# Kernel tuning notes

Hardware: AMD Instinct MI355X
Metric: run time of the kernel (lower is better)

The kernel has to match this reference:

```python
import jax, jax.numpy as jnp
import numpy as np

NUM_GRAPHS = 500


def setup_inputs() -> dict:
    key = jax.random.key(0)
    ks = jax.random.split(key, 8)
    num_nodes, feat, S, R, num_edges = 50000, 16, 128, 4, 1600000
    x = jax.random.normal(ks[0], (num_nodes, feat), dtype=jnp.float32)
    edge_index = jax.random.randint(ks[1], (2, num_edges), 0, num_nodes, dtype=jnp.int64)
    batch = jnp.sort(jax.random.randint(ks[2], (num_nodes,), 0, NUM_GRAPHS, dtype=jnp.int64))
    # ensure num_graphs == NUM_GRAPHS deterministically
    batch = batch.at[-1].set(NUM_GRAPHS - 1)
    scale = 1.0 / np.sqrt(S)
    W_msg = jax.random.uniform(ks[3], (R, S, S), jnp.float32, -scale, scale)
    b_msg = jax.random.uniform(ks[4], (R, S), jnp.float32, -scale, scale)
    W_upd = jax.random.uniform(ks[5], (R, S, S), jnp.float32, -scale, scale)
    b_upd = jax.random.uniform(ks[6], (R, S), jnp.float32, -scale, scale)
    return {"x": x, "W_msg": W_msg, "b_msg": b_msg, "W_upd": W_upd, "b_upd": b_upd,
            "edge_index": edge_index, "batch": batch}


def reference(x, W_msg, b_msg, W_upd, b_upd, edge_index, batch):
    num_nodes = x.shape[0]
    R, S, _ = W_msg.shape
    src, dst = edge_index[0], edge_index[1]
    # Original torch code initializes state to zeros (input_net is unused in forward).
    state = jnp.zeros((num_nodes, S), dtype=x.dtype)
    for r in range(R):
        message = jax.nn.relu(state @ W_msg[r].T + b_msg[r])          # [N, S]
        gathered = message[src]                                        # [E, S] gather
        agg = jnp.zeros((num_nodes, S), dtype=x.dtype).at[dst].add(gathered)  # scatter-add
        state = state + jax.nn.relu(agg @ W_upd[r].T + b_upd[r])
    graph_state = jax.ops.segment_sum(state, batch, num_segments=NUM_GRAPHS)  # [G, S]
    return graph_state
```

## Files before the change

kernel.cpp:

```cpp
#include <hip/hip_runtime.h>
#include <hip/hip_bf16.h>
#include <cstdint>
#include <cstddef>

#define SDIM 128
#define EPB2 4096
#define BCAP 4608

typedef short bf16x8 __attribute__((ext_vector_type(8)));
typedef float f32x4 __attribute__((ext_vector_type(4)));

__device__ __forceinline__ unsigned short f2bf(float f) {
  unsigned int u = __float_as_uint(f);
  unsigned int r = (u + 0x7FFF + ((u >> 16) & 1)) >> 16;
  return (unsigned short)r;
}
__device__ __forceinline__ float bf2f(unsigned short b) {
  return __uint_as_float(((unsigned int)b) << 16);
}

__global__ __launch_bounds__(256) void bucket_k(const int* __restrict__ src,
                                                const int* __restrict__ dst,
                                                int* __restrict__ bcursor,
                                                unsigned int* __restrict__ pairBuf4,
                                                int E) {
  __shared__ unsigned int s_buf[EPB2];
  __shared__ int cnt[512], base[512], gbase[512];
  const int tid = threadIdx.x;
  const int e0 = blockIdx.x * EPB2;
  const int n = min(EPB2, E - e0);
  cnt[tid] = 0; cnt[tid + 256] = 0;
  __syncthreads();

  unsigned int pack_r[16];
  int rank_r[16], bkt_r[16];
  if (n == EPB2) {
    const int4* dp = (const int4*)(dst + e0 + tid * 16);
    const int4* sp = (const int4*)(src + e0 + tid * 16);
#pragma unroll
    for (int q = 0; q < 4; ++q) {
      const int4 dv = dp[q];
      const int4 sv = sp[q];
      const int dd[4] = {dv.x, dv.y, dv.z, dv.w};
      const int ss[4] = {sv.x, sv.y, sv.z, sv.w};
#pragma unroll
      for (int w = 0; w < 4; ++w) {
        const int u = q * 4 + w;
        const int b = dd[w] >> 7;
        bkt_r[u] = b;
        pack_r[u] = ((unsigned int)dd[w] << 16) | (unsigned int)ss[w];
        rank_r[u] = atomicAdd(&cnt[b], 1);
      }
    }
  } else {
#pragma unroll
    for (int u = 0; u < 16; ++u) {
      const int li = u * 256 + tid;
      bkt_r[u] = -1;
      if (li < n) {
        const int i = e0 + li;
        const int d = dst[i];
        const int b = d >> 7;
        bkt_r[u] = b;
        pack_r[u] = ((unsigned int)d << 16) | (unsigned int)src[i];
        rank_r[u] = atomicAdd(&cnt[b], 1);
      }
    }
  }
  __syncthreads();
  if (tid < 64) {
    int carry = 0;
#pragma unroll
    for (int chunk = 0; chunk < 512; chunk += 256) {
      const int j0 = chunk + tid * 4;
      const int c0 = cnt[j0], c1 = cnt[j0 + 1], c2 = cnt[j0 + 2], c3 = cnt[j0 + 3];
      const int s = c0 + c1 + c2 + c3;
      int incl = s;
#pragma unroll
      for (int off = 1; off < 64; off <<= 1) {
        int u = __shfl_up(incl, off, 64);
        if (tid >= off) incl += u;
      }
      const int e = carry + incl - s;
      base[j0] = e;
      base[j0 + 1] = e + c0;
      base[j0 + 2] = e + c0 + c1;
      base[j0 + 3] = e + c0 + c1 + c2;
      carry += __shfl(incl, 63, 64);
    }
  }
  __syncthreads();
  for (int b = tid; b < 512; b += 256)
    if (cnt[b] > 0) gbase[b] = atomicAdd(&bcursor[b], cnt[b]);
  __syncthreads();
#pragma unroll
  for (int u = 0; u < 16; ++u) {
    if (n == EPB2 || bkt_r[u] >= 0)
      s_buf[base[bkt_r[u]] + rank_r[u]] = pack_r[u];
  }
  __syncthreads();
  for (int i = tid; i < n; i += 256) {
    const unsigned int p = s_buf[i];
    const int b = (int)(p >> 23);
    pairBuf4[(size_t)b * BCAP + (size_t)(gbase[b] + (i - base[b]))] = p;
  }
}

__global__ __launch_bounds__(512) void fill3_k(const unsigned int* __restrict__ pairBuf4,
                                               const int* __restrict__ bcursor,
                                               int* __restrict__ offs,
                                               int* __restrict__ oend,
                                               unsigned short* __restrict__ csr, int N) {
  const int b = blockIdx.x;
  const int rlo = b * BCAP;
  const int rhi = rlo + bcursor[b];
  const int lo_node = b << 7;
  __shared__ int hist[128], cur[128];
  const int tid = threadIdx.x;
  if (tid < 128) hist[tid] = 0;
  __syncthreads();
  for (int i = rlo + tid; i < rhi; i += 512)
    atomicAdd(&hist[(pairBuf4[i] >> 16) & 127], 1);
  __syncthreads();
  if (tid < 64) {
    const int j0 = tid * 2;
    const int h0 = hist[j0], h1 = hist[j0 + 1];
    const int s = h0 + h1;
    int incl = s;
#pragma unroll
    for (int off = 1; off < 64; off <<= 1) {
      int u = __shfl_up(incl, off, 64);
      if (tid >= off) incl += u;
    }
    const int e = rlo + incl - s;
    cur[j0] = e; cur[j0 + 1] = e + h0;
    const int n0 = lo_node + j0;
    if (n0 < N) { offs[n0] = e; oend[n0] = e + h0; }
    if (n0 + 1 < N) { offs[n0 + 1] = e + h0; oend[n0 + 1] = e + h0 + h1; }
  }
  __syncthreads();
  for (int i = rlo + tid; i < rhi; i += 512) {
    const unsigned int p = pairBuf4[i];
    const int pos = atomicAdd(&cur[(p >> 16) & 127], 1);
    csr[pos] = (unsigned short)p;
  }
}

__global__ __launch_bounds__(256) void cast2c_k(const float* __restrict__ a,
                                                const float* __restrict__ b,
                                                unsigned short* __restrict__ out, int n,
                                                const float* __restrict__ W_upd0,
                                                const float* __restrict__ b_msg0,
                                                float* __restrict__ cvec, int nCast) {
  if ((int)blockIdx.x == nCast) {
    __shared__ float m0[SDIM];
    const int j = threadIdx.x;
    if (j < SDIM) m0[j] = fmaxf(b_msg0[j], 0.f);
    __syncthreads();
    if (j < SDIM) {
      float s = 0.f;
      const float* wr = W_upd0 + (size_t)j * SDIM;
      for (int k = 0; k < SDIM; ++k) s += wr[k] * m0[k];
      cvec[j] = s;
    }
    return;
  }
  int i = (blockIdx.x * 256 + threadIdx.x) * 4;
  if (i >= 2 * n) return;
  const float* s = (i < n) ? (a + i) : (b + (i - n));
  float4 v = *(const float4*)s;
  ushort4 o;
  o.x = f2bf(v.x); o.y = f2bf(v.y); o.z = f2bf(v.z); o.w = f2bf(v.w);
  *(ushort4*)(out + i) = o;
}

__global__ __launch_bounds__(256) void initmsg_k(const int* __restrict__ offs,
                                                 const int* __restrict__ oend,
                                                 const float* __restrict__ cvec,
                                                 const float* __restrict__ bu0,
                                                 const unsigned short* __restrict__ Wm,
                                                 const float* __restrict__ bm,
                                                 unsigned short* __restrict__ sbf,
                                                 unsigned short* __restrict__ msgb, int N) {
  __shared__ unsigned short sT[4][16][136];
  const int tid = threadIdx.x, lane = tid & 63, wid = tid >> 6;
  const int r0 = blockIdx.x * 64 + wid * 16;
  int arow = r0 + (lane & 15);
  const bool rowOk = arow < N;
  if (!rowOk) arow = N - 1;
  const int kb = (lane >> 4) * 8;
  const float dn = (float)(oend[arow] - offs[arow]);

  bf16x8 a[4];
#pragma unroll
  for (int ks = 0; ks < 4; ++ks) {
    const int c0 = ks * 32 + kb;
#pragma unroll
    for (int q = 0; q < 8; ++q) {
      const float v = fmaxf(dn * cvec[c0 + q] + bu0[c0 + q], 0.f);
      a[ks][q] = (short)f2bf(v);
    }
    if (rowOk) *(bf16x8*)(sbf + (size_t)arow * SDIM + c0) = a[ks];
  }

  f32x4 acc[8];
#pragma unroll
  for (int jt = 0; jt < 8; ++jt) acc[jt] = (f32x4){0.f, 0.f, 0.f, 0.f};
  const int wrow = lane & 15;
#pragma unroll
  for (int ks = 0; ks < 4; ++ks) {
#pragma unroll
    for (int jt = 0; jt < 8; ++jt) {
      bf16x8 b = *(const bf16x8*)(Wm + (size_t)(jt * 16 + wrow) * SDIM + ks * 32 + kb);
      acc[jt] = __builtin_amdgcn_mfma_f32_16x16x32_bf16(a[ks], b, acc[jt], 0, 0, 0);
    }
  }
  const int colw = lane & 15;
  const int rt0 = (lane >> 4) * 4;
#pragma unroll
  for (int jt = 0; jt < 8; ++jt) {
    const float bj = bm[jt * 16 + colw];
#pragma unroll
    for (int r = 0; r < 4; ++r)
      sT[wid][rt0 + r][jt * 16 + colw] = f2bf(fmaxf(acc[jt][r] + bj, 0.f));
  }
  __syncthreads();
  const int vr = lane >> 4;
  const int vc = (lane & 15) * 8;
#pragma unroll
  for (int it = 0; it < 4; ++it) {
    const int lr = it * 4 + vr;
    const int row = r0 + lr;
    if (row < N)
      *(bf16x8*)(msgb + (size_t)row * SDIM + vc) = *(const bf16x8*)&sT[wid][lr][vc];
  }
}

template <bool MSG>
__global__ __launch_bounds__(256) void updmsg_k(const unsigned short* __restrict__ aggb,
                                                const unsigned short* __restrict__ Wu,
                                                const float* __restrict__ bu,
                                                unsigned short* __restrict__ sbf,
                                                const unsigned short* __restrict__ Wm,
                                                const float* __restrict__ bm,
                                                unsigned short* __restrict__ msgb, int N) {
  __shared__ unsigned short sT[4][16][136];
  const int tid = threadIdx.x, lane = tid & 63, wid = tid >> 6;
  const int r0 = blockIdx.x * 64 + wid * 16;
  int arow = r0 + (lane & 15);
  if (arow >= N) arow = N - 1;
  const int kb = (lane >> 4) * 8;

  f32x4 acc[8];
#pragma unroll
  for (int jt = 0; jt < 8; ++jt) acc[jt] = (f32x4){0.f, 0.f, 0.f, 0.f};
  bf16x8 a[4];
#pragma unroll
  for (int ks = 0; ks < 4; ++ks)
    a[ks] = *(const bf16x8*)(aggb + (size_t)arow * SDIM + ks * 32 + kb);
  const int wrow = lane & 15;
#pragma unroll
  for (int ks = 0; ks < 4; ++ks) {
#pragma unroll
    for (int jt = 0; jt < 8; ++jt) {
      bf16x8 b = *(const bf16x8*)(Wu + (size_t)(jt * 16 + wrow) * SDIM + ks * 32 + kb);
      acc[jt] = __builtin_amdgcn_mfma_f32_16x16x32_bf16(a[ks], b, acc[jt], 0, 0, 0);
    }
  }

  const int colw = lane & 15;
  const int rt0 = (lane >> 4) * 4;
#pragma unroll
  for (int jt = 0; jt < 8; ++jt) {
    const float bj = bu[jt * 16 + colw];
#pragma unroll
    for (int r = 0; r < 4; ++r)
      sT[wid][rt0 + r][jt * 16 + colw] = f2bf(fmaxf(acc[jt][r] + bj, 0.f));
  }
  __syncthreads();

  const int vr = lane >> 4;
  const int vc = (lane & 15) * 8;
#pragma unroll
  for (int it = 0; it < 4; ++it) {
    const int lr = it * 4 + vr;
    const int row = r0 + lr;
    if (row < N) {
      bf16x8 nw = *(const bf16x8*)&sT[wid][lr][vc];
      bf16x8 old = *(const bf16x8*)(sbf + (size_t)row * SDIM + vc);
      bf16x8 up;
#pragma unroll
      for (int q = 0; q < 8; ++q)
        up[q] = (short)f2bf(bf2f((unsigned short)old[q]) + bf2f((unsigned short)nw[q]));
      *(bf16x8*)(sbf + (size_t)row * SDIM + vc) = up;
      if (MSG) *(bf16x8*)&sT[wid][lr][vc] = up;
    }
  }

  if (MSG) {
    __syncthreads();
    f32x4 acc2[8];
#pragma unroll
    for (int jt = 0; jt < 8; ++jt) acc2[jt] = (f32x4){0.f, 0.f, 0.f, 0.f};
#pragma unroll
    for (int ks = 0; ks < 4; ++ks) {
      bf16x8 a2 = *(const bf16x8*)&sT[wid][lane & 15][ks * 32 + kb];
#pragma unroll
      for (int jt = 0; jt < 8; ++jt) {
        bf16x8 b = *(const bf16x8*)(Wm + (size_t)(jt * 16 + wrow) * SDIM + ks * 32 + kb);
        acc2[jt] = __builtin_amdgcn_mfma_f32_16x16x32_bf16(a2, b, acc2[jt], 0, 0, 0);
      }
    }
    __syncthreads();
#pragma unroll
    for (int jt = 0; jt < 8; ++jt) {
      const float bj = bm[jt * 16 + colw];
#pragma unroll
      for (int r = 0; r < 4; ++r)
        sT[wid][rt0 + r][jt * 16 + colw] = f2bf(fmaxf(acc2[jt][r] + bj, 0.f));
    }
    __syncthreads();
#pragma unroll
    for (int it = 0; it < 4; ++it) {
      const int lr = it * 4 + vr;
      const int row = r0 + lr;
      if (row < N)
        *(bf16x8*)(msgb + (size_t)row * SDIM + vc) = *(const bf16x8*)&sT[wid][lr][vc];
    }
  }
}

__global__ __launch_bounds__(256) void agg_bf16_k(const unsigned short* __restrict__ msg,
                                                  const unsigned short* __restrict__ csr,
                                                  const int* __restrict__ offs,
                                                  const int* __restrict__ oend,
                                                  unsigned short* __restrict__ aggb, int N) {
  const int wid = (blockIdx.x * 256 + threadIdx.x) >> 6;
  if (wid >= N) return;
  const int lane = threadIdx.x & 63;
  const int grp = lane >> 4;
  const unsigned int lb = (unsigned int)((lane & 15) << 4);
  const char* base = (const char*)msg;
  const int e1 = oend[wid];
  int e = offs[wid];
  float a0 = 0.f, a1 = 0.f, a2 = 0.f, a3 = 0.f, a4 = 0.f, a5 = 0.f, a6 = 0.f, a7 = 0.f;
#define ACC8(v) { \
  a0 += __uint_as_float((v).x << 16); a1 += __uint_as_float((v).x & 0xFFFF0000u); \
  a2 += __uint_as_float((v).y << 16); a3 += __uint_as_float((v).y & 0xFFFF0000u); \
  a4 += __uint_as_float((v).z << 16); a5 += __uint_as_float((v).z & 0xFFFF0000u); \
  a6 += __uint_as_float((v).w << 16); a7 += __uint_as_float((v).w & 0xFFFF0000u); }
  for (; e + 16 <= e1; e += 16) {
    const unsigned int o0 = ((unsigned int)csr[e + grp] << 8) | lb;
    const unsigned int o1 = ((unsigned int)csr[e + 4 + grp] << 8) | lb;
    const unsigned int o2 = ((unsigned int)csr[e + 8 + grp] << 8) | lb;
    const unsigned int o3 = ((unsigned int)csr[e + 12 + grp] << 8) | lb;
    uint4 vA = *(const uint4*)(base + o0);
    uint4 vB = *(const uint4*)(base + o1);
    uint4 vC = *(const uint4*)(base + o2);
    uint4 vD = *(const uint4*)(base + o3);
    ACC8(vA) ACC8(vB) ACC8(vC) ACC8(vD)
  }
  for (; e + 4 <= e1; e += 4) {
    const unsigned int o0 = ((unsigned int)csr[e + grp] << 8) | lb;
    uint4 v = *(const uint4*)(base + o0);
    ACC8(v)
  }
  if (e + grp < e1) {
    const unsigned int o0 = ((unsigned int)csr[e + grp] << 8) | lb;
    uint4 v = *(const uint4*)(base + o0);
    ACC8(v)
  }
#undef ACC8
#define RED(x) x += __shfl_xor(x, 16, 64); x += __shfl_xor(x, 32, 64);
  RED(a0) RED(a1) RED(a2) RED(a3) RED(a4) RED(a5) RED(a6) RED(a7)
#undef RED
  if (grp == 0) {
    uint4 o;
    o.x = (unsigned int)f2bf(a0) | ((unsigned int)f2bf(a1) << 16);
    o.y = (unsigned int)f2bf(a2) | ((unsigned int)f2bf(a3) << 16);
    o.z = (unsigned int)f2bf(a4) | ((unsigned int)f2bf(a5) << 16);
    o.w = (unsigned int)f2bf(a6) | ((unsigned int)f2bf(a7) << 16);
    *(uint4*)(aggb + ((size_t)wid << 7) + (lb >> 1)) = o;
  }
}

__global__ __launch_bounds__(SDIM) void segsum_k(const unsigned short* __restrict__ sbf,
                                                 const int* __restrict__ batch,
                                                 int N, float* __restrict__ out) {
  const int g = blockIdx.x;
  __shared__ int se[2];
  if (threadIdx.x < 2) {
    const int target = g + threadIdx.x;
    int lo = 0, hi = N;
    while (lo < hi) {
      const int mid = (lo + hi) >> 1;
      if (batch[mid] < target) lo = mid + 1; else hi = mid;
    }
    se[threadIdx.x] = lo;
  }
  __syncthreads();
  const int s = se[0], e = se[1];
  const int j = threadIdx.x;
  float acc = 0.f;
  for (int i = s; i < e; ++i) acc += bf2f(sbf[(size_t)i * SDIM + j]);
  out[(size_t)g * SDIM + j] = acc;
}

extern "C" void kernel_launch(void* const* d_in, const int* in_sizes, int n_in,
                              void* d_out, int out_size, void* d_ws, size_t ws_size,
                              hipStream_t stream) {
  const float* W_msg = (const float*)d_in[1];
  const float* b_msg = (const float*)d_in[2];
  const float* W_upd = (const float*)d_in[3];
  const float* b_upd = (const float*)d_in[4];
  const int* edges = (const int*)d_in[5];
  const int* batch = (const int*)d_in[6];
  const int E = in_sizes[5] / 2;
  const int N = in_sizes[6];
  const int G = out_size / SDIM;
  const int R = in_sizes[2] / SDIM;
  const int WSZ = R * SDIM * SDIM;

  const int NB = (N + 127) >> 7;

  const size_t NS = (size_t)N * SDIM;
  unsigned short* sbf = (unsigned short*)d_ws;
  unsigned short* msgb = sbf + NS;
  unsigned short* aggb = msgb + NS;
  unsigned short* wmsgb = aggb + NS;
  unsigned short* wupdb = wmsgb + WSZ;
  float* cvec = (float*)(wupdb + WSZ);
  int* offs = (int*)(cvec + SDIM);
  int* oend = offs + N;
  int* bcursor = oend + N;
  unsigned int* pairBuf4 = (unsigned int*)(bcursor + NB);
  unsigned short* csr = (unsigned short*)(pairBuf4 + (size_t)NB * BCAP);

  const int* srcArr = edges;
  const int* dstArr = edges + E;

  hipMemsetAsync(bcursor, 0, sizeof(int) * (size_t)NB, stream);

  const int nCast = (2 * WSZ / 4 + 255) / 256;
  cast2c_k<<<nCast + 1, 256, 0, stream>>>(W_msg, W_upd, wmsgb, WSZ,
                                          W_upd, b_msg, cvec, nCast);
  bucket_k<<<(E + EPB2 - 1) / EPB2, 256, 0, stream>>>(srcArr, dstArr, bcursor,
                                                      pairBuf4, E);
  fill3_k<<<NB, 512, 0, stream>>>(pairBuf4, bcursor, offs, oend, csr, N);

  const int gemmGrid = (N + 63) / 64;
  const int aggGrid = (N * 64 + 255) / 256;

  initmsg_k<<<gemmGrid, 256, 0, stream>>>(offs, oend, cvec, b_upd,
                                          wmsgb + (size_t)1 * SDIM * SDIM,
                                          b_msg + 1 * SDIM, sbf, msgb, N);
  agg_bf16_k<<<aggGrid, 256, 0, stream>>>(msgb, csr, offs, oend, aggb, N);
  for (int r = 1; r < R - 1; ++r) {
    updmsg_k<true><<<gemmGrid, 256, 0, stream>>>(
        aggb, wupdb + (size_t)r * SDIM * SDIM, b_upd + (size_t)r * SDIM, sbf,
        wmsgb + (size_t)(r + 1) * SDIM * SDIM, b_msg + (size_t)(r + 1) * SDIM, msgb, N);
    agg_bf16_k<<<aggGrid, 256, 0, stream>>>(msgb, csr, offs, oend, aggb, N);
  }
  updmsg_k<false><<<gemmGrid, 256, 0, stream>>>(
      aggb, wupdb + (size_t)(R - 1) * SDIM * SDIM, b_upd + (size_t)(R - 1) * SDIM, sbf,
      nullptr, nullptr, nullptr, N);

  segsum_k<<<G, SDIM, 0, stream>>>(sbf, batch, N, (float*)d_out);
}
```

Before: 340.2 us.

## Replace wavefront-per-node aggregation with thread-per-node column-sliced gather

The CSR gather-sum kernel changes from one 64-lane wavefront per destination node to one thread per node per 32-column slice. Each block handles one of four column slices and one half of the node range, and each thread keeps 32 fp32 accumulators in registers. This drops the cross-lane shuffle reduction and the index reads repeated across lane groups, and keeps each block's reads inside a 64-byte slice of the message rows, which may improve cache locality. In exchange, neighbouring lanes follow independent neighbour lists, so loads become uncoalesced and lanes diverge on uneven degrees, and register pressure rises.

Result: slower. 532.8 us (+56.6%).

```diff
diff --git a/kernel.cpp b/kernel.cpp
--- a/kernel.cpp
+++ b/kernel.cpp
@@ -330,57 +330,59 @@
   }
 }
 
-__global__ __launch_bounds__(256) void agg_bf16_k(const unsigned short* __restrict__ msg,
-                                                  const unsigned short* __restrict__ csr,
-                                                  const int* __restrict__ offs,
-                                                  const int* __restrict__ oend,
-                                                  unsigned short* __restrict__ aggb, int N) {
-  const int wid = (blockIdx.x * 256 + threadIdx.x) >> 6;
-  if (wid >= N) return;
-  const int lane = threadIdx.x & 63;
-  const int grp = lane >> 4;
-  const unsigned int lb = (unsigned int)((lane & 15) << 4);
-  const char* base = (const char*)msg;
-  const int e1 = oend[wid];
-  int e = offs[wid];
-  float a0 = 0.f, a1 = 0.f, a2 = 0.f, a3 = 0.f, a4 = 0.f, a5 = 0.f, a6 = 0.f, a7 = 0.f;
-#define ACC8(v) { \
-  a0 += __uint_as_float((v).x << 16); a1 += __uint_as_float((v).x & 0xFFFF0000u); \
-  a2 += __uint_as_float((v).y << 16); a3 += __uint_as_float((v).y & 0xFFFF0000u); \
-  a4 += __uint_as_float((v).z << 16); a5 += __uint_as_float((v).z & 0xFFFF0000u); \
-  a6 += __uint_as_float((v).w << 16); a7 += __uint_as_float((v).w & 0xFFFF0000u); }
-  for (; e + 16 <= e1; e += 16) {
-    const unsigned int o0 = ((unsigned int)csr[e + grp] << 8) | lb;
-    const unsigned int o1 = ((unsigned int)csr[e + 4 + grp] << 8) | lb;
-    const unsigned int o2 = ((unsigned int)csr[e + 8 + grp] << 8) | lb;
-    const unsigned int o3 = ((unsigned int)csr[e + 12 + grp] << 8) | lb;
-    uint4 vA = *(const uint4*)(base + o0);
-    uint4 vB = *(const uint4*)(base + o1);
-    uint4 vC = *(const uint4*)(base + o2);
-    uint4 vD = *(const uint4*)(base + o3);
-    ACC8(vA) ACC8(vB) ACC8(vC) ACC8(vD)
-  }
-  for (; e + 4 <= e1; e += 4) {
-    const unsigned int o0 = ((unsigned int)csr[e + grp] << 8) | lb;
-    uint4 v = *(const uint4*)(base + o0);
-    ACC8(v)
-  }
-  if (e + grp < e1) {
-    const unsigned int o0 = ((unsigned int)csr[e + grp] << 8) | lb;
-    uint4 v = *(const uint4*)(base + o0);
-    ACC8(v)
-  }
-#undef ACC8
-#define RED(x) x += __shfl_xor(x, 16, 64); x += __shfl_xor(x, 32, 64);
-  RED(a0) RED(a1) RED(a2) RED(a3) RED(a4) RED(a5) RED(a6) RED(a7)
-#undef RED
-  if (grp == 0) {
+__global__ __launch_bounds__(256) void agg_slice_k(const unsigned short* __restrict__ msg,
+                                                   const unsigned short* __restrict__ csr,
+                                                   const int* __restrict__ offs,
+                                                   const int* __restrict__ oend,
+                                                   unsigned short* __restrict__ aggb,
+                                                   int N, int Nhalf) {
+  const int xs = blockIdx.x & 7;
+  const int colSlice = xs >> 1;
+  const int half = xs & 1;
+  const int nb = blockIdx.x >> 3;
+  const int lo = half * Nhalf;
+  const int hi = min(N, lo + Nhalf);
+  const int node = lo + nb * 256 + (int)threadIdx.x;
+  if (node >= hi) return;
+
+  const int e0 = offs[node], e1 = oend[node];
+  const char* base = (const char*)msg + colSlice * 64;
+
+  float acc[32];
+#pragma unroll
+  for (int q = 0; q < 32; ++q) acc[q] = 0.f;
+
+#define ADD8(v, o) { \
+  acc[o + 0] += __uint_as_float((v).x << 16); acc[o + 1] += __uint_as_float((v).x & 0xFFFF0000u); \
+  acc[o + 2] += __uint_as_float((v).y << 16); acc[o + 3] += __uint_as_float((v).y & 0xFFFF0000u); \
+  acc[o + 4] += __uint_as_float((v).z << 16); acc[o + 5] += __uint_as_float((v).z & 0xFFFF0000u); \
+  acc[o + 6] += __uint_as_float((v).w << 16); acc[o + 7] += __uint_as_float((v).w & 0xFFFF0000u); }
+
+  int e = e0;
+  for (; e + 2 <= e1; e += 2) {
+    const uint4* pA = (const uint4*)(base + ((size_t)csr[e] << 8));
+    const uint4* pB = (const uint4*)(base + ((size_t)csr[e + 1] << 8));
+    uint4 a0 = pA[0], a1 = pA[1], a2 = pA[2], a3 = pA[3];
+    uint4 b0 = pB[0], b1 = pB[1], b2 = pB[2], b3 = pB[3];
+    ADD8(a0, 0) ADD8(a1, 8) ADD8(a2, 16) ADD8(a3, 24)
+    ADD8(b0, 0) ADD8(b1, 8) ADD8(b2, 16) ADD8(b3, 24)
+  }
+  if (e < e1) {
+    const uint4* pA = (const uint4*)(base + ((size_t)csr[e] << 8));
+    uint4 a0 = pA[0], a1 = pA[1], a2 = pA[2], a3 = pA[3];
+    ADD8(a0, 0) ADD8(a1, 8) ADD8(a2, 16) ADD8(a3, 24)
+  }
+#undef ADD8
+
+  unsigned short* drow = aggb + (size_t)node * SDIM + colSlice * 32;
+#pragma unroll
+  for (int v = 0; v < 4; ++v) {
     uint4 o;
-    o.x = (unsigned int)f2bf(a0) | ((unsigned int)f2bf(a1) << 16);
-    o.y = (unsigned int)f2bf(a2) | ((unsigned int)f2bf(a3) << 16);
-    o.z = (unsigned int)f2bf(a4) | ((unsigned int)f2bf(a5) << 16);
-    o.w = (unsigned int)f2bf(a6) | ((unsigned int)f2bf(a7) << 16);
-    *(uint4*)(aggb + ((size_t)wid << 7) + (lb >> 1)) = o;
+    o.x = (unsigned int)f2bf(acc[v * 8 + 0]) | ((unsigned int)f2bf(acc[v * 8 + 1]) << 16);
+    o.y = (unsigned int)f2bf(acc[v * 8 + 2]) | ((unsigned int)f2bf(acc[v * 8 + 3]) << 16);
+    o.z = (unsigned int)f2bf(acc[v * 8 + 4]) | ((unsigned int)f2bf(acc[v * 8 + 5]) << 16);
+    o.w = (unsigned int)f2bf(acc[v * 8 + 6]) | ((unsigned int)f2bf(acc[v * 8 + 7]) << 16);
+    *(uint4*)(drow + v * 8) = o;
   }
 }
 
@@ -449,17 +451,18 @@
   fill3_k<<<NB, 512, 0, stream>>>(pairBuf4, bcursor, offs, oend, csr, N);
 
   const int gemmGrid = (N + 63) / 64;
-  const int aggGrid = (N * 64 + 255) / 256;
+  const int Nhalf = (N + 1) / 2;
+  const int aggGrid = ((Nhalf + 255) / 256) * 8;
 
   initmsg_k<<<gemmGrid, 256, 0, stream>>>(offs, oend, cvec, b_upd,
                                           wmsgb + (size_t)1 * SDIM * SDIM,
                                           b_msg + 1 * SDIM, sbf, msgb, N);
-  agg_bf16_k<<<aggGrid, 256, 0, stream>>>(msgb, csr, offs, oend, aggb, N);
+  agg_slice_k<<<aggGrid, 256, 0, stream>>>(msgb, csr, offs, oend, aggb, N, Nhalf);
   for (int r = 1; r < R - 1; ++r) {
     updmsg_k<true><<<gemmGrid, 256, 0, stream>>>(
         aggb, wupdb + (size_t)r * SDIM * SDIM, b_upd + (size_t)r * SDIM, sbf,
         wmsgb + (size_t)(r + 1) * SDIM * SDIM, b_msg + (size_t)(r + 1) * SDIM, msgb, N);
-    agg_bf16_k<<<aggGrid, 256, 0, stream>>>(msgb, csr, offs, oend, aggb, N);
+    agg_slice_k<<<aggGrid, 256, 0, stream>>>(msgb, csr, offs, oend, aggb, N, Nhalf);
   }
   updmsg_k<false><<<gemmGrid, 256, 0, stream>>>(
       aggb, wupdb + (size_t)(R - 1) * SDIM * SDIM, b_upd + (size_t)(R - 1) * SDIM, sbf,
```
